# Kernel tuning notes

Measured on AMD Instinct MI355X. Metric: run time of the kernel, lower is better.

Reference implementation:

```python
import jax, jax.numpy as jnp
import numpy as np
import math

T = 2048
D_MODEL = 2048
N_H = 16
D_H = D_MODEL // N_H
EPS = 1e-5


def _rope_tables(t, d_h):
    # standard RoPE cos/sin tables, full head-dim layout matching rotate_half
    inv_freq = 1.0 / (10000.0 ** (jnp.arange(0, d_h // 2, dtype=jnp.float32) / (d_h // 2)))
    ang = jnp.arange(t, dtype=jnp.float32)[:, None] * inv_freq[None, :]  # (T, d_h/2)
    ang = jnp.concatenate([ang, ang], axis=-1)  # (T, d_h)
    return jnp.cos(ang), jnp.sin(ang)


def setup_inputs() -> dict:
    key = jax.random.key(0)
    kx, kq, kk, kv, ko = jax.random.split(key, 5)
    scale = 1.0 / math.sqrt(D_MODEL)
    cos, sin = _rope_tables(T, D_H)
    return {
        "x": jax.random.normal(kx, (T, D_MODEL), dtype=jnp.float32),
        "cos": cos,
        "sin": sin,
        "attention_mask": jnp.ones((T,), dtype=jnp.int32),
        "ln_w": jnp.ones((D_MODEL,), dtype=jnp.float32),
        "Wq": jax.random.normal(kq, (D_MODEL, D_MODEL), dtype=jnp.float32) * scale,
        "Wk": jax.random.normal(kk, (D_MODEL, D_MODEL), dtype=jnp.float32) * scale,
        "Wv": jax.random.normal(kv, (D_MODEL, D_MODEL), dtype=jnp.float32) * scale,
        "Wo": jax.random.normal(ko, (D_MODEL, D_MODEL), dtype=jnp.float32) * scale,
    }


def _rotate_half(x):
    x1, x2 = jnp.split(x, 2, axis=-1)
    return jnp.concatenate((-x2, x1), axis=-1)


def reference(x, cos, sin, attention_mask, ln_w, Wq, Wk, Wv, Wo):
    t = x.shape[0]
    # RMSNorm
    var = jnp.mean(x * x, axis=-1, keepdims=True)
    h = ln_w * x * jax.lax.rsqrt(var + EPS)
    # QKV projections (eqx Linear: weight @ x => x @ W.T), reshape to (n_h, T, d_h)
    q = (h @ Wq.T).reshape(t, N_H, D_H).transpose(1, 0, 2)
    k = (h @ Wk.T).reshape(t, N_H, D_H).transpose(1, 0, 2)
    v = (h @ Wv.T).reshape(t, N_H, D_H).transpose(1, 0, 2)
    # RoPE (cos/sin broadcast (T,d_h) -> (n_h,T,d_h))
    q = q * cos + _rotate_half(q) * sin
    k = k * cos + _rotate_half(k) * sin
    scores = jnp.einsum('hqd,hkd->hqk', q, k) / math.sqrt(D_H)
    causal = jnp.tril(jnp.ones((t, t), dtype=bool))[None]
    neg = jnp.finfo(scores.dtype).min
    am = attention_mask.astype(bool)
    allowed = causal & am[None, None, :]
    scores = jnp.where(allowed, scores, neg)
    scores = jnp.where(am[None, :, None], scores, neg)
    probs = jax.nn.softmax(scores, axis=-1)
    out = jnp.einsum('hqk,hkd->hqd', probs, v).transpose(1, 0, 2).reshape(t, -1)
    out = out @ Wo.T
    out = jnp.where(am[:, None], out, 0.0)
    return x + out
```

## Files before the change

### kernel.cpp

```cpp
#include <hip/hip_runtime.h>
#include <stdint.h>

#define TS 2048
#define DM 2048
#define NH 16
#define DH 128

typedef unsigned short u16t;
typedef __attribute__((ext_vector_type(8))) short short8;
typedef __attribute__((ext_vector_type(4))) float f32x4;
typedef __attribute__((ext_vector_type(4))) unsigned int u32x4;
typedef __attribute__((ext_vector_type(4))) unsigned short u16x4;

__device__ __forceinline__ float bf2f(u16t b) {
  return __uint_as_float(((unsigned int)b) << 16);
}
__device__ __forceinline__ u16t f2bf(float f) {
  unsigned int u = __float_as_uint(f);
  u += 0x7FFFu + ((u >> 16) & 1u);
  return (u16t)(u >> 16);
}

__device__ __forceinline__ void async_copy16(const u16t* g, u16t* l) {
  __builtin_amdgcn_global_load_lds((const __attribute__((address_space(1))) void*)g,
                                   (__attribute__((address_space(3))) void*)l, 16, 0, 0);
}

#define DPP_ROR_F(x, n) __uint_as_float(__builtin_amdgcn_update_dpp( \
    0, (int)__float_as_uint(x), 0x120 | (n), 0xF, 0xF, true))

__device__ __forceinline__ float row16_max(float x) {
  x = fmaxf(x, DPP_ROR_F(x, 8));
  x = fmaxf(x, DPP_ROR_F(x, 4));
  x = fmaxf(x, DPP_ROR_F(x, 2));
  x = fmaxf(x, DPP_ROR_F(x, 1));
  return x;
}
__device__ __forceinline__ float row16_sum(float x) {
  x += DPP_ROR_F(x, 8);
  x += DPP_ROR_F(x, 4);
  x += DPP_ROR_F(x, 2);
  x += DPP_ROR_F(x, 1);
  return x;
}

__global__ __launch_bounds__(256) void cast_rms_kernel(const float* __restrict__ W0,
                                                       const float* __restrict__ W1,
                                                       const float* __restrict__ W2,
                                                       const float* __restrict__ W3,
                                                       u16t* __restrict__ outw,
                                                       const float* __restrict__ x,
                                                       const float* __restrict__ lnw,
                                                       u16t* __restrict__ h) {
  if (blockIdx.x < 16384) {
    const int idx = blockIdx.x * 256 + threadIdx.x;
    const int mat = idx >> 20;
    const size_t off = (size_t)(idx & 0xFFFFF) * 4;
    const float* W = (mat == 0) ? W0 : (mat == 1) ? W1 : (mat == 2) ? W2 : W3;
    const f32x4 v = *(const f32x4*)(W + off);
    size_t dstoff = off;
    if (mat < 2) {
      const int row = (int)(off >> 11);
      const int col = (int)(off & 2047);
      const int d = row & 127;
      const int e = d & 63;
      const int p = ((e >> 4) * 32 + (e & 15)) + ((d >> 6) << 4);
      dstoff = ((size_t)((row & ~127) | p) << 11) | (size_t)col;
    }
    union { u16t s[4]; uint64_t u; } o;
#pragma unroll
    for (int i = 0; i < 4; ++i) o.s[i] = f2bf(v[i]);
    *(uint64_t*)(outw + (size_t)mat * (DM * DM) + dstoff) = o.u;
    return;
  }
  const int row = blockIdx.x - 16384;
  const int tid = threadIdx.x;
  const float* xr = x + (size_t)row * DM + tid * 8;
  f32x4 v0 = *(const f32x4*)(xr);
  f32x4 v1 = *(const f32x4*)(xr + 4);
  float f[8];
#pragma unroll
  for (int i = 0; i < 4; ++i) { f[i] = v0[i]; f[i + 4] = v1[i]; }
  float ss = 0.f;
#pragma unroll
  for (int i = 0; i < 8; ++i) ss += f[i] * f[i];
#pragma unroll
  for (int off = 1; off < 64; off <<= 1) ss += __shfl_xor(ss, off, 64);
  __shared__ float wsum[4];
  if ((tid & 63) == 0) wsum[tid >> 6] = ss;
  __syncthreads();
  float tot = wsum[0] + wsum[1] + wsum[2] + wsum[3];
  float rs = rsqrtf(tot * (1.0f / DM) + 1e-5f);
  f32x4 w0 = *(const f32x4*)(lnw + tid * 8);
  f32x4 w1 = *(const f32x4*)(lnw + tid * 8 + 4);
  u32x4 o;
#pragma unroll
  for (int i = 0; i < 4; ++i) {
    unsigned int lo = f2bf(f[2 * i]     * ((2 * i     < 4) ? w0[2 * i]     : w1[2 * i - 4]) * rs);
    unsigned int hi = f2bf(f[2 * i + 1] * ((2 * i + 1 < 4) ? w0[2 * i + 1] : w1[2 * i - 3]) * rs);
    o[i] = lo | (hi << 16);
  }
  *(u32x4*)(h + (size_t)row * DM + tid * 8) = o;
}

template <int MODE>
__global__ __launch_bounds__(512, 2) void gemm8(
    const u16t* __restrict__ A,
    const u16t* __restrict__ B0, const u16t* __restrict__ B1, const u16t* __restrict__ B2,
    u16t* __restrict__ Cq, u16t* __restrict__ Ck, u16t* __restrict__ Cv,
    u16t* __restrict__ P0, u16t* __restrict__ P1,
    u16t* __restrict__ P2, u16t* __restrict__ P3,
    const float* __restrict__ cosb, const float* __restrict__ sinb) {
  __shared__ u16t Ab[2][256 * 64];
  __shared__ u16t Bb[2][256 * 64];
  const int tid  = threadIdx.x;
  const int wave = tid >> 6;
  const int lane = tid & 63;
  const int quad = lane >> 4;
  const int c16  = lane & 15;
  const int h7   = c16 & 7;
  const int wm   = wave >> 2;
  const int wn   = wave & 3;
  const int nwg  = gridDim.x;
  const int bid  = blockIdx.x;
  const int wgid = (bid & 7) * (nwg >> 3) + (bid >> 3);
  const int mat  = wgid >> 6;
  const int rem  = wgid & 63;
  const int m0   = (rem & 7) * 256;
  const int n0   = ((rem >> 3) & 7) * 256;
  const u16t* B  = (MODE == 0) ? (mat == 0 ? B0 : (mat == 1 ? B1 : B2)) : B0;
  const int kbeg = (MODE == 0) ? 0 : mat * (DM / 4);
  const int NT   = (MODE == 0) ? (DM / 64) : (DM / 4 / 64);

  const int srow = lane >> 3;
  const int sg   = (lane & 7) ^ srow;
  auto stage = [&](int d, int k0) {
    const size_t koff = (size_t)k0 + sg * 8;
#pragma unroll
    for (int c = 0; c < 4; ++c) {
      const int rb = wave * 32 + c * 8;
      async_copy16(A + (size_t)(m0 + rb + srow) * DM + koff, &Ab[d][rb * 64]);
      async_copy16(B + (size_t)(n0 + rb + srow) * DM + koff, &Bb[d][rb * 64]);
    }
  };

  const f32x4 fzero = {0.f, 0.f, 0.f, 0.f};
  f32x4 acc[8][4];
#pragma unroll
  for (int i = 0; i < 8; ++i)
#pragma unroll
    for (int j = 0; j < 4; ++j) acc[i][j] = fzero;

  stage(0, kbeg);
  asm volatile("s_waitcnt vmcnt(0)" ::: "memory");
  __builtin_amdgcn_s_barrier();

  for (int kt = 0; kt < NT; ++kt) {
    const int cur = kt & 1;
    if (kt + 1 < NT) stage(cur ^ 1, kbeg + (kt + 1) * 64);
    const u16t* Abuf = Ab[cur];
    const u16t* Bbuf = Bb[cur];
    __builtin_amdgcn_s_setprio(1);
#pragma unroll
    for (int ks = 0; ks < 2; ++ks) {
      short8 af[8], bfr[4];
#pragma unroll
      for (int i = 0; i < 8; ++i) {
        const int row = wm * 128 + i * 16 + c16;
        af[i] = *(const short8*)(Abuf + row * 64 + (((ks * 4 + quad) ^ h7) * 8));
      }
#pragma unroll
      for (int nt = 0; nt < 4; ++nt) {
        const int row = wn * 64 + nt * 16 + c16;
        bfr[nt] = *(const short8*)(Bbuf + row * 64 + (((ks * 4 + quad) ^ h7) * 8));
      }
#pragma unroll
      for (int i = 0; i < 8; ++i)
#pragma unroll
        for (int nt = 0; nt < 4; ++nt)
          acc[i][nt] =
              __builtin_amdgcn_mfma_f32_16x16x32_bf16(af[i], bfr[nt], acc[i][nt], 0, 0, 0);
    }
    __builtin_amdgcn_s_setprio(0);
    asm volatile("s_waitcnt vmcnt(0)" ::: "memory");
    __builtin_amdgcn_s_barrier();
  }

  if (MODE == 1) {
    u16t* P = (mat == 0) ? P0 : (mat == 1) ? P1 : (mat == 2) ? P2 : P3;
#pragma unroll
    for (int mt = 0; mt < 8; ++mt) {
#pragma unroll
      for (int r = 0; r < 4; ++r) {
        const int row = m0 + wm * 128 + mt * 16 + quad * 4 + r;
        const size_t base = (size_t)row * DM;
#pragma unroll
        for (int nt = 0; nt < 4; ++nt) {
          const int col = n0 + wn * 64 + nt * 16 + c16;
          P[base + col] = f2bf(acc[mt][nt][r]);
        }
      }
    }
    return;
  }
  if (mat == 2) {
#pragma unroll
    for (int mt = 0; mt < 8; ++mt) {
#pragma unroll
      for (int r = 0; r < 4; ++r) {
        const int row = m0 + wm * 128 + mt * 16 + quad * 4 + r;
#pragma unroll
        for (int nt = 0; nt < 4; ++nt) {
          const int col = n0 + wn * 64 + nt * 16 + c16;
          Cv[(size_t)col * TS + row] = f2bf(acc[mt][nt][r]);
        }
      }
    }
    return;
  }
  u16t* C = mat ? Ck : Cq;
#pragma unroll
  for (int mt = 0; mt < 8; ++mt) {
#pragma unroll
    for (int r = 0; r < 4; ++r) {
      const int row = m0 + wm * 128 + mt * 16 + quad * 4 + r;
      const size_t base = (size_t)row * DM;
#pragma unroll
      for (int ntp = 0; ntp < 4; ntp += 2) {
        const int col = n0 + wn * 64 + ntp * 16 + c16;
        const int p = col & 127;
        const int dorig = ((p >> 5) << 4) + c16;
        const float cv = cosb[row * DH + dorig];
        const float sv = sinb[row * DH + dorig];
        const float x1 = acc[mt][ntp][r];
        const float x2 = acc[mt][ntp + 1][r];
        C[base + col]      = f2bf(x1 * cv - x2 * sv);
        C[base + col + 16] = f2bf(x2 * cv + x1 * sv);
      }
    }
  }
}

__global__ __launch_bounds__(256) void combine4_kernel(const u16t* __restrict__ P0,
                                                       const u16t* __restrict__ P1,
                                                       const u16t* __restrict__ P2,
                                                       const u16t* __restrict__ P3,
                                                       const float* __restrict__ x,
                                                       const int* __restrict__ am,
                                                       float* __restrict__ out) {
  const size_t idx = ((size_t)blockIdx.x * 256 + threadIdx.x) * 4;
  const int row = (int)(idx >> 11);
  const float mk = (am[row] != 0) ? 1.f : 0.f;
  const u16x4 a = *(const u16x4*)(P0 + idx);
  const u16x4 b = *(const u16x4*)(P1 + idx);
  const u16x4 c = *(const u16x4*)(P2 + idx);
  const u16x4 d = *(const u16x4*)(P3 + idx);
  const f32x4 xr = *(const f32x4*)(x + idx);
  f32x4 o;
#pragma unroll
  for (int i = 0; i < 4; ++i)
    o[i] = xr[i] + mk * ((bf2f(a[i]) + bf2f(b[i])) + (bf2f(c[i]) + bf2f(d[i])));
  *(f32x4*)(out + idx) = o;
}

__global__ __launch_bounds__(256) void attn_kernel(const u16t* __restrict__ Q,
                                                   const u16t* __restrict__ K,
                                                   const u16t* __restrict__ Vt,
                                                   const int* __restrict__ am,
                                                   u16t* __restrict__ O) {
  __shared__ u16t Klds[128 * 128];
  __shared__ u16t Vlds[128 * 128];
  __shared__ u16t Plds[4][2048];
  const int wave = threadIdx.x >> 6;
  const int lane = threadIdx.x & 63;
  const int x    = blockIdx.x;
  const int half = x >> 8;
  const int idx  = x & 255;
  const int head = idx & (NH - 1);
  const int grp  = idx >> 4;
  const int qt   = half ? grp : (TS / 64 - 1 - grp);
  const int q0   = qt * 64 + wave * 16;
  const int quad = lane >> 4;
  const int c16  = lane & 15;
  const u16t* Qh  = Q + head * DH;
  const u16t* Kh  = K + head * DH;
  const u16t* Vth = Vt + (size_t)head * DH * TS;
  u16t* Pw = Plds[wave];

  const int row_s = (lane >> 4);
  const int g_s   = (lane & 15);

  short8 qf[4];
#pragma unroll
  for (int dc = 0; dc < 4; ++dc)
    qf[dc] = *(const short8*)(Qh + (size_t)(q0 + c16) * DM + dc * 32 + quad * 8);

  const f32x4 fzero = {0.f, 0.f, 0.f, 0.f};
  float m_run[4], l_run[4];
  f32x4 o_acc[8];
#pragma unroll
  for (int r = 0; r < 4; ++r) { m_run[r] = -1e30f; l_run[r] = 0.f; }
#pragma unroll
  for (int nt = 0; nt < 8; ++nt) o_acc[nt] = fzero;

  const float scale = 0.08838834764831845f;
  const int ntiles = (qt * 64 + 191) >> 7;

  for (int kt = 0; kt < ntiles; ++kt) {
    const int k0 = kt * 128;
    __syncthreads();
#pragma unroll
    for (int c = 0; c < 8; ++c) {
      const int ch = wave * 8 + c;
      const int r  = 4 * ch + row_s;
      const int g  = g_s ^ (r & 15);
      async_copy16(Kh + (size_t)(k0 + r) * DM + g * 8, Klds + ch * 512);
      async_copy16(Vth + (size_t)r * TS + k0 + g * 8, Vlds + ch * 512);
    }
    __syncthreads();

    f32x4 s[8];
#pragma unroll
    for (int ns = 0; ns < 8; ++ns) {
      f32x4 sa = fzero;
      const int rr = ns * 16 + c16;
#pragma unroll
      for (int dc = 0; dc < 4; ++dc) {
        short8 kf = *(const short8*)(Klds + rr * 128 + (((dc * 4 + quad) ^ c16) * 8));
        sa = __builtin_amdgcn_mfma_f32_16x16x32_bf16(qf[dc], kf, sa, 0, 0, 0);
      }
      s[ns] = sa;
    }

    float pv[8][4], tmax[4];
#pragma unroll
    for (int r = 0; r < 4; ++r) tmax[r] = -1e30f;
#pragma unroll
    for (int ns = 0; ns < 8; ++ns) {
      const int key = k0 + ns * 16 + c16;
      const bool kok = (am[key] != 0);
#pragma unroll
      for (int r = 0; r < 4; ++r) {
        const int qrow = q0 + quad * 4 + r;
        float v = s[ns][r] * scale;
        if (key > qrow || !kok) v = -1e30f;
        pv[ns][r] = v;
        tmax[r] = fmaxf(tmax[r], v);
      }
    }
    float alpha[4], rsum[4];
#pragma unroll
    for (int r = 0; r < 4; ++r) {
      const float mn = fmaxf(m_run[r], row16_max(tmax[r]));
      alpha[r] = __expf(m_run[r] - mn);
      m_run[r] = mn;
      float rs = 0.f;
#pragma unroll
      for (int ns = 0; ns < 8; ++ns) {
        const float e = __expf(pv[ns][r] - mn);
        pv[ns][r] = e;
        rs += e;
      }
      rsum[r] = row16_sum(rs);
      l_run[r] = l_run[r] * alpha[r] + rsum[r];
    }

#pragma unroll
    for (int ns = 0; ns < 8; ++ns)
#pragma unroll
      for (int r = 0; r < 4; ++r)
        Pw[(ns >> 1) * 512 + (quad * 4 + r) * 32 + (ns & 1) * 16 + c16] = f2bf(pv[ns][r]);
    asm volatile("s_waitcnt lgkmcnt(0)" ::: "memory");
    short8 pf[4];
#pragma unroll
    for (int c = 0; c < 4; ++c)
      pf[c] = *(const short8*)(Pw + c * 512 + c16 * 32 + quad * 8);

#pragma unroll
    for (int nt = 0; nt < 8; ++nt)
#pragma unroll
      for (int r = 0; r < 4; ++r) o_acc[nt][r] *= alpha[r];
#pragma unroll
    for (int nt = 0; nt < 8; ++nt) {
      const int rr = nt * 16 + c16;
#pragma unroll
      for (int c = 0; c < 4; ++c) {
        short8 vf = *(const short8*)(Vlds + rr * 128 + (((c * 4 + quad) ^ c16) * 8));
        o_acc[nt] = __builtin_amdgcn_mfma_f32_16x16x32_bf16(pf[c], vf, o_acc[nt], 0, 0, 0);
      }
    }
  }

#pragma unroll
  for (int r = 0; r < 4; ++r) {
    const float inv = 1.0f / fmaxf(l_run[r], 1e-20f);
    const int qrow = q0 + quad * 4 + r;
#pragma unroll
    for (int nt = 0; nt < 8; ++nt)
      O[(size_t)qrow * DM + head * DH + nt * 16 + c16] = f2bf(o_acc[nt][r] * inv);
  }
}

extern "C" void kernel_launch(void* const* d_in, const int* in_sizes, int n_in,
                              void* d_out, int out_size, void* d_ws, size_t ws_size,
                              hipStream_t stream) {
  const float* x    = (const float*)d_in[0];
  const float* cosb = (const float*)d_in[1];
  const float* sinb = (const float*)d_in[2];
  const int*   am   = (const int*)d_in[3];
  const float* lnw  = (const float*)d_in[4];
  const float* Wq   = (const float*)d_in[5];
  const float* Wk   = (const float*)d_in[6];
  const float* Wv   = (const float*)d_in[7];
  const float* Wo   = (const float*)d_in[8];
  float* out = (float*)d_out;

  u16t* h    = (u16t*)d_ws;
  u16t* Q    = h + (size_t)TS * DM;
  u16t* K    = Q + (size_t)TS * DM;
  u16t* Vt   = K + (size_t)TS * DM;
  u16t* attn = Vt + (size_t)TS * DM;
  u16t* Wb   = attn + (size_t)TS * DM;
  u16t* Wqb = Wb;
  u16t* Wkb = Wb + (size_t)DM * DM;
  u16t* Wvb = Wb + 2 * (size_t)DM * DM;
  u16t* Wob = Wb + 3 * (size_t)DM * DM;

  cast_rms_kernel<<<16384 + TS, 256, 0, stream>>>(Wq, Wk, Wv, Wo, Wb, x, lnw, h);
  gemm8<0><<<192, 512, 0, stream>>>(h, Wqb, Wkb, Wvb, Q, K, Vt,
                                    nullptr, nullptr, nullptr, nullptr, cosb, sinb);
  attn_kernel<<<NH * (TS / 64), 256, 0, stream>>>(Q, K, Vt, am, attn);
  gemm8<1><<<256, 512, 0, stream>>>(attn, Wob, nullptr, nullptr,
                                    nullptr, nullptr, nullptr,
                                    h, Q, K, Vt, nullptr, nullptr);
  combine4_kernel<<<(TS * DM / 4) / 256, 256, 0, stream>>>(h, Q, K, Vt, x, am, out);
}
```

Measured before the change: 292.2 us.

## Fuse Q/K/V projections into one 128x128 tile GEMM sharing A tiles

Replaces the 192-block QKV GEMM (256x256 tiles, one weight matrix per block) with a 256-block kernel where each block computes a 128x128 output tile for all three of Q, K and V. The block stages one A tile and reuses it across the three weight matrices. This is meant to fill all 256 CUs on the device instead of leaving some idle with 192 blocks. The cost is less reuse per tile, since the accumulators cover 3x4x2 fragments per wave, and more global traffic for B relative to compute. The output projection GEMM is split into its own non-templated kernel with unchanged behavior.

```diff
diff --git a/kernel.cpp b/kernel.cpp
--- a/kernel.cpp
+++ b/kernel.cpp
@@ -103,14 +103,123 @@
   *(u32x4*)(h + (size_t)row * DM + tid * 8) = o;
 }
 
-template <int MODE>
-__global__ __launch_bounds__(512, 2) void gemm8(
+__global__ __launch_bounds__(512, 2) void gemm_qkv(
     const u16t* __restrict__ A,
     const u16t* __restrict__ B0, const u16t* __restrict__ B1, const u16t* __restrict__ B2,
     u16t* __restrict__ Cq, u16t* __restrict__ Ck, u16t* __restrict__ Cv,
+    const float* __restrict__ cosb, const float* __restrict__ sinb) {
+  __shared__ u16t Ab[2][128 * 64];
+  __shared__ u16t Bb[3][2][128 * 64];
+  const int tid  = threadIdx.x;
+  const int wave = tid >> 6;
+  const int lane = tid & 63;
+  const int quad = lane >> 4;
+  const int c16  = lane & 15;
+  const int h7   = c16 & 7;
+  const int wm   = wave >> 2;
+  const int wn   = wave & 3;
+  const int bid  = blockIdx.x;
+  const int wgid = (bid & 7) * 32 + (bid >> 3);
+  const int m0   = (wgid & 15) * 128;
+  const int n0   = (wgid >> 4) * 128;
+
+  const int srow = lane >> 3;
+  const int sg   = (lane & 7) ^ srow;
+  auto stage = [&](int d, int k0) {
+    const size_t koff = (size_t)k0 + sg * 8;
+#pragma unroll
+    for (int c = 0; c < 2; ++c) {
+      const int rb = wave * 16 + c * 8;
+      async_copy16(A  + (size_t)(m0 + rb + srow) * DM + koff, &Ab[d][rb * 64]);
+      async_copy16(B0 + (size_t)(n0 + rb + srow) * DM + koff, &Bb[0][d][rb * 64]);
+      async_copy16(B1 + (size_t)(n0 + rb + srow) * DM + koff, &Bb[1][d][rb * 64]);
+      async_copy16(B2 + (size_t)(n0 + rb + srow) * DM + koff, &Bb[2][d][rb * 64]);
+    }
+  };
+
+  const f32x4 fzero = {0.f, 0.f, 0.f, 0.f};
+  f32x4 acc[3][4][2];
+#pragma unroll
+  for (int m = 0; m < 3; ++m)
+#pragma unroll
+    for (int i = 0; i < 4; ++i)
+#pragma unroll
+      for (int j = 0; j < 2; ++j) acc[m][i][j] = fzero;
+
+  stage(0, 0);
+  asm volatile("s_waitcnt vmcnt(0)" ::: "memory");
+  __builtin_amdgcn_s_barrier();
+
+  for (int kt = 0; kt < DM / 64; ++kt) {
+    const int cur = kt & 1;
+    if (kt + 1 < DM / 64) stage(cur ^ 1, (kt + 1) * 64);
+    const u16t* Abuf = Ab[cur];
+    __builtin_amdgcn_s_setprio(1);
+#pragma unroll
+    for (int ks = 0; ks < 2; ++ks) {
+      const int gsw = ((ks * 4 + quad) ^ h7) * 8;
+      short8 af[4], bfr[3][2];
+#pragma unroll
+      for (int i = 0; i < 4; ++i)
+        af[i] = *(const short8*)(Abuf + (wm * 64 + i * 16 + c16) * 64 + gsw);
+#pragma unroll
+      for (int m = 0; m < 3; ++m)
+#pragma unroll
+        for (int nt = 0; nt < 2; ++nt)
+          bfr[m][nt] = *(const short8*)(&Bb[m][cur][0] + (wn * 32 + nt * 16 + c16) * 64 + gsw);
+#pragma unroll
+      for (int m = 0; m < 3; ++m)
+#pragma unroll
+        for (int i = 0; i < 4; ++i)
+#pragma unroll
+          for (int nt = 0; nt < 2; ++nt)
+            acc[m][i][nt] =
+                __builtin_amdgcn_mfma_f32_16x16x32_bf16(af[i], bfr[m][nt], acc[m][i][nt], 0, 0, 0);
+    }
+    __builtin_amdgcn_s_setprio(0);
+    asm volatile("s_waitcnt vmcnt(0)" ::: "memory");
+    __builtin_amdgcn_s_barrier();
+  }
+
+#pragma unroll
+  for (int mat = 0; mat < 2; ++mat) {
+    u16t* C = mat ? Ck : Cq;
+#pragma unroll
+    for (int mt = 0; mt < 4; ++mt) {
+#pragma unroll
+      for (int r = 0; r < 4; ++r) {
+        const int row = m0 + wm * 64 + mt * 16 + quad * 4 + r;
+        const size_t base = (size_t)row * DM;
+        const int col = n0 + wn * 32 + c16;
+        const int p = col & 127;
+        const int dorig = ((p >> 5) << 4) + c16;
+        const float cv = cosb[row * DH + dorig];
+        const float sv = sinb[row * DH + dorig];
+        const float x1 = acc[mat][mt][0][r];
+        const float x2 = acc[mat][mt][1][r];
+        C[base + col]      = f2bf(x1 * cv - x2 * sv);
+        C[base + col + 16] = f2bf(x2 * cv + x1 * sv);
+      }
+    }
+  }
+#pragma unroll
+  for (int mt = 0; mt < 4; ++mt) {
+#pragma unroll
+    for (int r = 0; r < 4; ++r) {
+      const int row = m0 + wm * 64 + mt * 16 + quad * 4 + r;
+#pragma unroll
+      for (int nt = 0; nt < 2; ++nt) {
+        const int col = n0 + wn * 32 + nt * 16 + c16;
+        Cv[(size_t)col * TS + row] = f2bf(acc[2][mt][nt][r]);
+      }
+    }
+  }
+}
+
+__global__ __launch_bounds__(512, 2) void gemm_out(
+    const u16t* __restrict__ A, const u16t* __restrict__ B0,
     u16t* __restrict__ P0, u16t* __restrict__ P1,
-    u16t* __restrict__ P2, u16t* __restrict__ P3,
-    const float* __restrict__ cosb, const float* __restrict__ sinb) {
+    u16t* __restrict__ P2, u16t* __restrict__ P3) {
   __shared__ u16t Ab[2][256 * 64];
   __shared__ u16t Bb[2][256 * 64];
   const int tid  = threadIdx.x;
@@ -128,9 +237,8 @@
   const int rem  = wgid & 63;
   const int m0   = (rem & 7) * 256;
   const int n0   = ((rem >> 3) & 7) * 256;
-  const u16t* B  = (MODE == 0) ? (mat == 0 ? B0 : (mat == 1 ? B1 : B2)) : B0;
-  const int kbeg = (MODE == 0) ? 0 : mat * (DM / 4);
-  const int NT   = (MODE == 0) ? (DM / 64) : (DM / 4 / 64);
+  const int kbeg = mat * (DM / 4);
+  const int NT   = DM / 4 / 64;
 
   const int srow = lane >> 3;
   const int sg   = (lane & 7) ^ srow;
@@ -140,7 +248,7 @@
     for (int c = 0; c < 4; ++c) {
       const int rb = wave * 32 + c * 8;
       async_copy16(A + (size_t)(m0 + rb + srow) * DM + koff, &Ab[d][rb * 64]);
-      async_copy16(B + (size_t)(n0 + rb + srow) * DM + koff, &Bb[d][rb * 64]);
+      async_copy16(B0 + (size_t)(n0 + rb + srow) * DM + koff, &Bb[d][rb * 64]);
     }
   };
 
@@ -186,39 +294,7 @@
     __builtin_amdgcn_s_barrier();
   }
 
-  if (MODE == 1) {
-    u16t* P = (mat == 0) ? P0 : (mat == 1) ? P1 : (mat == 2) ? P2 : P3;
-#pragma unroll
-    for (int mt = 0; mt < 8; ++mt) {
-#pragma unroll
-      for (int r = 0; r < 4; ++r) {
-        const int row = m0 + wm * 128 + mt * 16 + quad * 4 + r;
-        const size_t base = (size_t)row * DM;
-#pragma unroll
-        for (int nt = 0; nt < 4; ++nt) {
-          const int col = n0 + wn * 64 + nt * 16 + c16;
-          P[base + col] = f2bf(acc[mt][nt][r]);
-        }
-      }
-    }
-    return;
-  }
-  if (mat == 2) {
-#pragma unroll
-    for (int mt = 0; mt < 8; ++mt) {
-#pragma unroll
-      for (int r = 0; r < 4; ++r) {
-        const int row = m0 + wm * 128 + mt * 16 + quad * 4 + r;
-#pragma unroll
-        for (int nt = 0; nt < 4; ++nt) {
-          const int col = n0 + wn * 64 + nt * 16 + c16;
-          Cv[(size_t)col * TS + row] = f2bf(acc[mt][nt][r]);
-        }
-      }
-    }
-    return;
-  }
-  u16t* C = mat ? Ck : Cq;
+  u16t* P = (mat == 0) ? P0 : (mat == 1) ? P1 : (mat == 2) ? P2 : P3;
 #pragma unroll
   for (int mt = 0; mt < 8; ++mt) {
 #pragma unroll
@@ -226,16 +302,9 @@
       const int row = m0 + wm * 128 + mt * 16 + quad * 4 + r;
       const size_t base = (size_t)row * DM;
 #pragma unroll
-      for (int ntp = 0; ntp < 4; ntp += 2) {
-        const int col = n0 + wn * 64 + ntp * 16 + c16;
-        const int p = col & 127;
-        const int dorig = ((p >> 5) << 4) + c16;
-        const float cv = cosb[row * DH + dorig];
-        const float sv = sinb[row * DH + dorig];
-        const float x1 = acc[mt][ntp][r];
-        const float x2 = acc[mt][ntp + 1][r];
-        C[base + col]      = f2bf(x1 * cv - x2 * sv);
-        C[base + col + 16] = f2bf(x2 * cv + x1 * sv);
+      for (int nt = 0; nt < 4; ++nt) {
+        const int col = n0 + wn * 64 + nt * 16 + c16;
+        P[base + col] = f2bf(acc[mt][nt][r]);
       }
     }
   }
@@ -427,11 +496,8 @@
   u16t* Wob = Wb + 3 * (size_t)DM * DM;
 
   cast_rms_kernel<<<16384 + TS, 256, 0, stream>>>(Wq, Wk, Wv, Wo, Wb, x, lnw, h);
-  gemm8<0><<<192, 512, 0, stream>>>(h, Wqb, Wkb, Wvb, Q, K, Vt,
-                                    nullptr, nullptr, nullptr, nullptr, cosb, sinb);
+  gemm_qkv<<<256, 512, 0, stream>>>(h, Wqb, Wkb, Wvb, Q, K, Vt, cosb, sinb);
   attn_kernel<<<NH * (TS / 64), 256, 0, stream>>>(Q, K, Vt, am, attn);
-  gemm8<1><<<256, 512, 0, stream>>>(attn, Wob, nullptr, nullptr,
-                                    nullptr, nullptr, nullptr,
-                                    h, Q, K, Vt, nullptr, nullptr);
+  gemm_out<<<256, 512, 0, stream>>>(attn, Wob, h, Q, K, Vt);
   combine4_kernel<<<(TS * DM / 4) / 256, 256, 0, stream>>>(h, Q, K, Vt, x, am, out);
 }
```

Result: faster. 281.3 us (-3.7%).
